# Optimization experiments

Hardware: AMD Instinct MI355X
Metric: run time of the kernel (lower is better)

The kernel has to match this reference:

```python
import jax, jax.numpy as jnp
import numpy as np

B, H, E, L = 2048, 4096, 8, 512
TAU = 1.0


def setup_inputs() -> dict:
    key = jax.random.key(0)
    k1, k2, k3, k4 = jax.random.split(key, 4)
    hidden = jax.random.normal(k1, (B, H), dtype=jnp.float32)
    envs = jax.random.normal(k2, (B, E), dtype=jnp.float32)
    idx = jnp.arange(B, dtype=jnp.int64)
    gumbel = jax.random.gumbel(k3, (B, E), dtype=jnp.float32)
    W = jax.random.normal(k4, (E, L, H), dtype=jnp.float32) * (1.0 / np.sqrt(H))
    return {"hidden": hidden, "envs": envs, "idx": idx, "gumbel": gumbel, "W": W}


def _hard_gumbel_softmax(log_probs, gumbel, tau):
    # F.gumbel_softmax(log_probs, tau=1, hard=True) with pre-sampled gumbel noise
    y_soft = jax.nn.softmax((log_probs + gumbel) / tau, axis=-1)
    y_hard = jax.nn.one_hot(jnp.argmax(y_soft, axis=-1), y_soft.shape[-1], dtype=y_soft.dtype)
    # straight-through estimator
    return y_hard + y_soft - jax.lax.stop_gradient(y_soft)


def reference(hidden, envs, idx, gumbel, W):
    # gating: env = gumbel_softmax(log_softmax(envs[idx]))  -> [B, E]
    log_probs = jax.nn.log_softmax(envs[idx], axis=-1)
    env = _hard_gumbel_softmax(log_probs, gumbel, TAU)
    # per-expert logits: [B, E, L]; fuses the per-sample python loop
    expert_logits = jnp.einsum("bh,elh->bel", hidden, W)
    # gating combine: [B, L]
    logits = jnp.einsum("be,bel->bl", env, expert_logits)
    # variance penalty over expert weights
    W_mean = jnp.mean(W, axis=0)  # [L, H]
    diff_sq = jnp.sum((W - W_mean[None]) ** 2, axis=(1, 2))  # ||W_e - W_mean||_2^2 per expert
    l1 = jnp.sum(jnp.abs(W), axis=(1, 2))                    # ||W_e||_1 per expert
    loss_penalty = jnp.mean(diff_sq / (l1 ** 2))
    return logits, loss_penalty
```

## Files before the change

kernel.cpp:

```cpp
#include <hip/hip_runtime.h>
#include <hip/hip_bf16.h>

constexpr int B = 2048, H = 4096, E = 8, L = 512;
constexpr int LH = L * H;

typedef float f4v __attribute__((ext_vector_type(4)));
typedef short short8 __attribute__((ext_vector_type(8)));

constexpr int BT = 128;
constexpr int LT = 128;
constexpr int KT = 32;
constexpr int SK = 4;
constexpr int RTMAX = 3;
constexpr int NITER = (H / SK) / KT;

constexpr int NGEMM = 4 * 2 * 4 * 4 * RTMAX;
constexpr int NPEN = 2048;

constexpr size_t WS_COUNTS = 0;
constexpr size_t WS_ACCUM = 32;
constexpr size_t WS_ROWLIST = 96;
constexpr size_t WS_ZERO_BYTES = 96;

using as1_u32 = const __attribute__((address_space(1))) unsigned int;
using as3_u32 = __attribute__((address_space(3))) unsigned int;

static __device__ __forceinline__ void dma16(const float* g, float* lds) {
  __builtin_amdgcn_global_load_lds((as1_u32*)g, (as3_u32*)lds, 16, 0, 0);
}

static __device__ __forceinline__ unsigned pk2(float a, float b) {
  __hip_bfloat162 p = __float22bfloat162_rn(make_float2(a, b));
  unsigned u;
  __builtin_memcpy(&u, &p, 4);
  return u;
}

static __device__ __forceinline__ short8 cvt8(f4v lo, f4v hi) {
  union { short8 s; unsigned u[4]; } r;
  r.u[0] = pk2(lo.x, lo.y);
  r.u[1] = pk2(lo.z, lo.w);
  r.u[2] = pk2(hi.x, hi.y);
  r.u[3] = pk2(hi.z, hi.w);
  return r.s;
}

__global__ void gating_kernel(const float* __restrict__ envs,
                              const float* __restrict__ gumbel,
                              int* __restrict__ counts,
                              int* __restrict__ row_list) {
  int b = blockIdx.x * blockDim.x + threadIdx.x;
  if (b >= B) return;
  float zmax = -1e30f;
  int am = 0;
#pragma unroll
  for (int e = 0; e < E; ++e) {
    float z = envs[b * E + e] + gumbel[b * E + e];
    if (z > zmax) { zmax = z; am = e; }
  }
  int pos = atomicAdd(&counts[am], 1);
  row_list[am * B + pos] = b;
}

__launch_bounds__(256, 2)
__global__ void fused_kernel(const float* __restrict__ hidden,
                             const float* __restrict__ W,
                             const int* __restrict__ counts,
                             const int* __restrict__ row_list,
                             float* __restrict__ out,
                             float* __restrict__ accum) {
  const int id = blockIdx.x;
  const int t = threadIdx.x;

  __shared__ __align__(16) float AshF[2][BT * KT];
  __shared__ __align__(16) float BshF[2][LT * KT];
  __shared__ int rlsh[BT];
  __shared__ float red[4][16];

  if (id >= NGEMM) {
    const int p = (id - NGEMM) * 256 + t;

    float4 w[E];
    float mx = 0.f, my = 0.f, mz = 0.f, mw = 0.f;
#pragma unroll
    for (int e = 0; e < E; ++e) {
      w[e] = *(const float4*)(W + (size_t)e * LH + (size_t)p * 4);
      mx += w[e].x; my += w[e].y; mz += w[e].z; mw += w[e].w;
    }
    mx *= 0.125f; my *= 0.125f; mz *= 0.125f; mw *= 0.125f;

    float vals[16];
#pragma unroll
    for (int e = 0; e < E; ++e) {
      float dx = w[e].x - mx, dy = w[e].y - my, dz = w[e].z - mz,
            dw = w[e].w - mw;
      vals[e] = dx * dx + dy * dy + dz * dz + dw * dw;
      vals[8 + e] =
          fabsf(w[e].x) + fabsf(w[e].y) + fabsf(w[e].z) + fabsf(w[e].w);
    }
#pragma unroll
    for (int k = 0; k < 16; ++k) {
      float v = vals[k];
      for (int off = 32; off > 0; off >>= 1) v += __shfl_xor(v, off);
      vals[k] = v;
    }
    const int wv = t >> 6, lane = t & 63;
    if (lane == 0) {
#pragma unroll
      for (int k = 0; k < 16; ++k) red[wv][k] = vals[k];
    }
    __syncthreads();
    if (t < 16) {
      atomicAdd(&accum[t], red[0][t] + red[1][t] + red[2][t] + red[3][t]);
    }
    return;
  }

  const int lt = id & 3;
  const int ep = (id >> 2) & 1;
  const int sk = (id >> 3) & 3;
  const int eh = (id >> 5) & 3;
  const int rt = id >> 7;
  const int e = eh * 2 + ep;

  const int cnt = counts[e];
  const int rbase = rt * BT;
  if (rbase >= cnt) return;
  const int lbase = lt * LT;

  if (t < BT) {
    int rr = rbase + t;
    rlsh[t] = row_list[e * B + (rr < cnt ? rr : (cnt - 1))];
  }
  __syncthreads();

  const float* Wp = W + (size_t)e * LH + (size_t)lbase * H;

  const int wave = t >> 6;
  const int lane = t & 63;
  const int quad = lane >> 4;
  const int l16 = lane & 15;
  const int wm = (wave >> 1) * 64;
  const int wn = (wave & 1) * 64;

  const int kbeg = sk * (H / SK);
  const int srow = lane >> 3;
  const int sblk = lane & 7;

  const float* sp[8];
  float* sl[2][8];
  const bool stageA = (wave < 2);
#pragma unroll
  for (int i = 0; i < 8; ++i) {
    int r = (stageA ? wave : (wave - 2)) * 64 + i * 8 + srow;
    int gblk = sblk ^ (r & 7);
    if (stageA) {
      sp[i] = hidden + (size_t)rlsh[r] * H + kbeg + gblk * 4;
      sl[0][i] = &AshF[0][(r - srow) * KT];
      sl[1][i] = &AshF[1][(r - srow) * KT];
    } else {
      sp[i] = Wp + (size_t)r * H + kbeg + gblk * 4;
      sl[0][i] = &BshF[0][(r - srow) * KT];
      sl[1][i] = &BshF[1][(r - srow) * KT];
    }
  }

  auto stage = [&](int buf) {
#pragma unroll
    for (int i = 0; i < 8; ++i) {
      dma16(sp[i], sl[buf][i]);
      sp[i] += KT;
    }
  };

  const int r7 = l16 & 7;
  const int slo = (2 * quad) ^ r7;
  const int shi = slo ^ 1;

  f4v acc[4][4] = {};

  stage(0);

  for (int it = 0; it < NITER; ++it) {
    const int buf = it & 1;
    __syncthreads();
    if (it + 1 < NITER) stage(buf ^ 1);

    short8 af[4], bf[4];
#pragma unroll
    for (int i = 0; i < 4; ++i) {
      int ra = wm + i * 16 + l16;
      f4v lo = *(const f4v*)&AshF[buf][ra * KT + slo * 4];
      f4v hi = *(const f4v*)&AshF[buf][ra * KT + shi * 4];
      af[i] = cvt8(lo, hi);
    }
#pragma unroll
    for (int j = 0; j < 4; ++j) {
      int rb = wn + j * 16 + l16;
      f4v lo = *(const f4v*)&BshF[buf][rb * KT + slo * 4];
      f4v hi = *(const f4v*)&BshF[buf][rb * KT + shi * 4];
      bf[j] = cvt8(lo, hi);
    }
#pragma unroll
    for (int i = 0; i < 4; ++i)
#pragma unroll
      for (int j = 0; j < 4; ++j)
        acc[i][j] =
            __builtin_amdgcn_mfma_f32_16x16x32_bf16(af[i], bf[j], acc[i][j],
                                                    0, 0, 0);
  }

#pragma unroll
  for (int i = 0; i < 4; ++i) {
#pragma unroll
    for (int j = 0; j < 4; ++j) {
#pragma unroll
      for (int reg = 0; reg < 4; ++reg) {
        int rloc = wm + i * 16 + quad * 4 + reg;
        if (rbase + rloc < cnt) {
          int bidx = rlsh[rloc];
          atomicAdd(&out[(size_t)bidx * L + lbase + wn + j * 16 + l16],
                    acc[i][j][reg]);
        }
      }
    }
  }
}

__global__ void finalize_kernel(const float* __restrict__ accum,
                                float* __restrict__ out) {
  if (threadIdx.x == 0) {
    float loss = 0.f;
#pragma unroll
    for (int e = 0; e < E; ++e) {
      float l1 = accum[8 + e];
      loss += accum[e] / (l1 * l1);
    }
    out[(size_t)B * L] = loss * 0.125f;
  }
}

extern "C" void kernel_launch(void* const* d_in, const int* in_sizes, int n_in,
                              void* d_out, int out_size, void* d_ws, size_t ws_size,
                              hipStream_t stream) {
  (void)in_sizes; (void)n_in; (void)ws_size;
  const float* hidden = (const float*)d_in[0];
  const float* envs   = (const float*)d_in[1];
  const float* gumbel = (const float*)d_in[3];
  const float* W      = (const float*)d_in[4];
  float* out = (float*)d_out;

  char* ws = (char*)d_ws;
  int*   counts   = (int*)(ws + WS_COUNTS);
  float* accum    = (float*)(ws + WS_ACCUM);
  int*   row_list = (int*)(ws + WS_ROWLIST);

  (void)hipMemsetAsync(d_ws, 0, WS_ZERO_BYTES, stream);
  (void)hipMemsetAsync(d_out, 0, (size_t)out_size * sizeof(float), stream);

  gating_kernel<<<dim3(B / 256), dim3(256), 0, stream>>>(envs, gumbel, counts,
                                                         row_list);

  fused_kernel<<<dim3(NGEMM + NPEN), dim3(256), 0, stream>>>(
      hidden, W, counts, row_list, out, accum);

  finalize_kernel<<<dim3(1), dim3(64), 0, stream>>>(accum, out);
}
```

Measured before the change: 180.8 us.

## Halve row tile, interleave GEMM and penalty blocks, raise occupancy

The row tile drops from 128 to 64 and the maximum row-tile count doubles, so expert GEMM work is split into finer blocks that pad less against the uneven per-expert row counts. GEMM blocks and the W-penalty reduction blocks are interleaved in a 3:8 pattern across the grid so both run at the same time instead of the penalty blocks trailing at the end. Launch bounds move to 3 blocks per SM with smaller accumulators, and the DMA staging is redistributed across all four waves. In exchange, each block reuses its W tile across fewer rows, which raises W traffic and the number of atomic adds to the output.

```diff
diff --git a/kernel.cpp b/kernel.cpp
--- a/kernel.cpp
+++ b/kernel.cpp
@@ -7,15 +7,17 @@
 typedef float f4v __attribute__((ext_vector_type(4)));
 typedef short short8 __attribute__((ext_vector_type(8)));
 
-constexpr int BT = 128;
+constexpr int BT = 64;
 constexpr int LT = 128;
 constexpr int KT = 32;
 constexpr int SK = 4;
-constexpr int RTMAX = 3;
+constexpr int RTMAX = 6;
 constexpr int NITER = (H / SK) / KT;
 
 constexpr int NGEMM = 4 * 2 * 4 * 4 * RTMAX;
 constexpr int NPEN = 2048;
+
+constexpr int NGRID = NGEMM + NPEN;
 
 constexpr size_t WS_COUNTS = 0;
 constexpr size_t WS_ACCUM = 32;
@@ -62,7 +64,7 @@
   row_list[am * B + pos] = b;
 }
 
-__launch_bounds__(256, 2)
+__launch_bounds__(256, 3)
 __global__ void fused_kernel(const float* __restrict__ hidden,
                              const float* __restrict__ W,
                              const int* __restrict__ counts,
@@ -77,8 +79,12 @@
   __shared__ int rlsh[BT];
   __shared__ float red[4][16];
 
-  if (id >= NGEMM) {
-    const int p = (id - NGEMM) * 256 + t;
+  const int grp = id / 11;
+  const int rem = id - grp * 11;
+  const bool is_gemm = (rem < 3);
+
+  if (!is_gemm) {
+    const int p = (grp * 8 + (rem - 3)) * 256 + t;
 
     float4 w[E];
     float mx = 0.f, my = 0.f, mz = 0.f, mw = 0.f;
@@ -116,11 +122,12 @@
     return;
   }
 
-  const int lt = id & 3;
-  const int ep = (id >> 2) & 1;
-  const int sk = (id >> 3) & 3;
-  const int eh = (id >> 5) & 3;
-  const int rt = id >> 7;
+  const int gidx = grp * 3 + rem;
+  const int lt = gidx & 3;
+  const int ep = (gidx >> 2) & 1;
+  const int sk = (gidx >> 3) & 3;
+  const int eh = (gidx >> 5) & 3;
+  const int rt = gidx >> 7;
   const int e = eh * 2 + ep;
 
   const int cnt = counts[e];
@@ -140,34 +147,35 @@
   const int lane = t & 63;
   const int quad = lane >> 4;
   const int l16 = lane & 15;
-  const int wm = (wave >> 1) * 64;
+  const int wm = (wave >> 1) * 32;
   const int wn = (wave & 1) * 64;
 
   const int kbeg = sk * (H / SK);
   const int srow = lane >> 3;
   const int sblk = lane & 7;
-
-  const float* sp[8];
-  float* sl[2][8];
-  const bool stageA = (wave < 2);
-#pragma unroll
-  for (int i = 0; i < 8; ++i) {
-    int r = (stageA ? wave : (wave - 2)) * 64 + i * 8 + srow;
-    int gblk = sblk ^ (r & 7);
-    if (stageA) {
-      sp[i] = hidden + (size_t)rlsh[r] * H + kbeg + gblk * 4;
-      sl[0][i] = &AshF[0][(r - srow) * KT];
-      sl[1][i] = &AshF[1][(r - srow) * KT];
+  const int gblk = sblk ^ srow;
+
+  const float* sp[6];
+  float* sl[2][6];
+#pragma unroll
+  for (int i = 0; i < 6; ++i) {
+    int g = wave * 6 + i;
+    if (g < 8) {
+      int rr = g * 8 + srow;
+      sp[i] = hidden + (size_t)rlsh[rr] * H + kbeg + gblk * 4;
+      sl[0][i] = &AshF[0][g * 8 * KT];
+      sl[1][i] = &AshF[1][g * 8 * KT];
     } else {
-      sp[i] = Wp + (size_t)r * H + kbeg + gblk * 4;
-      sl[0][i] = &BshF[0][(r - srow) * KT];
-      sl[1][i] = &BshF[1][(r - srow) * KT];
+      int rb = (g - 8) * 8 + srow;
+      sp[i] = Wp + (size_t)rb * H + kbeg + gblk * 4;
+      sl[0][i] = &BshF[0][(g - 8) * 8 * KT];
+      sl[1][i] = &BshF[1][(g - 8) * 8 * KT];
     }
   }
 
   auto stage = [&](int buf) {
 #pragma unroll
-    for (int i = 0; i < 8; ++i) {
+    for (int i = 0; i < 6; ++i) {
       dma16(sp[i], sl[buf][i]);
       sp[i] += KT;
     }
@@ -177,7 +185,7 @@
   const int slo = (2 * quad) ^ r7;
   const int shi = slo ^ 1;
 
-  f4v acc[4][4] = {};
+  f4v acc[2][4] = {};
 
   stage(0);
 
@@ -186,9 +194,9 @@
     __syncthreads();
     if (it + 1 < NITER) stage(buf ^ 1);
 
-    short8 af[4], bf[4];
-#pragma unroll
-    for (int i = 0; i < 4; ++i) {
+    short8 af[2], bf[4];
+#pragma unroll
+    for (int i = 0; i < 2; ++i) {
       int ra = wm + i * 16 + l16;
       f4v lo = *(const f4v*)&AshF[buf][ra * KT + slo * 4];
       f4v hi = *(const f4v*)&AshF[buf][ra * KT + shi * 4];
@@ -202,7 +210,7 @@
       bf[j] = cvt8(lo, hi);
     }
 #pragma unroll
-    for (int i = 0; i < 4; ++i)
+    for (int i = 0; i < 2; ++i)
 #pragma unroll
       for (int j = 0; j < 4; ++j)
         acc[i][j] =
@@ -211,7 +219,7 @@
   }
 
 #pragma unroll
-  for (int i = 0; i < 4; ++i) {
+  for (int i = 0; i < 2; ++i) {
 #pragma unroll
     for (int j = 0; j < 4; ++j) {
 #pragma unroll
@@ -261,8 +269,8 @@
   gating_kernel<<<dim3(B / 256), dim3(256), 0, stream>>>(envs, gumbel, counts,
                                                          row_list);
 
-  fused_kernel<<<dim3(NGEMM + NPEN), dim3(256), 0, stream>>>(
-      hidden, W, counts, row_list, out, accum);
+  fused_kernel<<<dim3(NGRID), dim3(256), 0, stream>>>(hidden, W, counts,
+                                                      row_list, out, accum);
 
   finalize_kernel<<<dim3(1), dim3(64), 0, stream>>>(accum, out);
 }
```

Result: slower. 195.1 us (+7.9%).

## Double split-K and interleave penalty blocks with GEMM blocks in grid

Applied to the files above, without the earlier changes.

Raises the split-K factor from 4 to 8, doubling the number of GEMM tiles and halving each tile's K loop. Penalty work moves into grid-stride blocks (1536 instead of 2048) that are interleaved 16-per-8 with GEMM blocks, so both kinds of block run at the same time instead of all penalty blocks being dispatched after the GEMM ones. The aim is better load balance and occupancy across CUs, since many GEMM blocks exit early when an expert has few rows. The cost is twice as many atomic adds into the output and a shorter pipeline in each block.

```diff
diff --git a/kernel.cpp b/kernel.cpp
--- a/kernel.cpp
+++ b/kernel.cpp
@@ -10,12 +10,13 @@
 constexpr int BT = 128;
 constexpr int LT = 128;
 constexpr int KT = 32;
-constexpr int SK = 4;
+constexpr int SK = 8;
 constexpr int RTMAX = 3;
 constexpr int NITER = (H / SK) / KT;
 
-constexpr int NGEMM = 4 * 2 * 4 * 4 * RTMAX;
-constexpr int NPEN = 2048;
+constexpr int NGEMM = 4 * 2 * 8 * 4 * RTMAX;
+constexpr int NPEN = 96 * 16;
+constexpr int NGRID = 96 * 24;
 
 constexpr size_t WS_COUNTS = 0;
 constexpr size_t WS_ACCUM = 32;
@@ -77,27 +78,38 @@
   __shared__ int rlsh[BT];
   __shared__ float red[4][16];
 
-  if (id >= NGEMM) {
-    const int p = (id - NGEMM) * 256 + t;
-
-    float4 w[E];
-    float mx = 0.f, my = 0.f, mz = 0.f, mw = 0.f;
-#pragma unroll
-    for (int e = 0; e < E; ++e) {
-      w[e] = *(const float4*)(W + (size_t)e * LH + (size_t)p * 4);
-      mx += w[e].x; my += w[e].y; mz += w[e].z; mw += w[e].w;
-    }
-    mx *= 0.125f; my *= 0.125f; mz *= 0.125f; mw *= 0.125f;
+  const int grp = id / 24;
+  const int rem = id - grp * 24;
+
+  if (rem >= 8) {
+    const int pidx = grp * 16 + (rem - 8);
+
+    float dacc[E], lacc[E];
+#pragma unroll
+    for (int e = 0; e < E; ++e) { dacc[e] = 0.f; lacc[e] = 0.f; }
+
+    for (int p = pidx * 256 + t; p < LH / 4; p += NPEN * 256) {
+      float4 w[E];
+      float mx = 0.f, my = 0.f, mz = 0.f, mw = 0.f;
+#pragma unroll
+      for (int e = 0; e < E; ++e) {
+        w[e] = *(const float4*)(W + (size_t)e * LH + (size_t)p * 4);
+        mx += w[e].x; my += w[e].y; mz += w[e].z; mw += w[e].w;
+      }
+      mx *= 0.125f; my *= 0.125f; mz *= 0.125f; mw *= 0.125f;
+#pragma unroll
+      for (int e = 0; e < E; ++e) {
+        float dx = w[e].x - mx, dy = w[e].y - my, dz = w[e].z - mz,
+              dw = w[e].w - mw;
+        dacc[e] += dx * dx + dy * dy + dz * dz + dw * dw;
+        lacc[e] +=
+            fabsf(w[e].x) + fabsf(w[e].y) + fabsf(w[e].z) + fabsf(w[e].w);
+      }
+    }
 
     float vals[16];
 #pragma unroll
-    for (int e = 0; e < E; ++e) {
-      float dx = w[e].x - mx, dy = w[e].y - my, dz = w[e].z - mz,
-            dw = w[e].w - mw;
-      vals[e] = dx * dx + dy * dy + dz * dz + dw * dw;
-      vals[8 + e] =
-          fabsf(w[e].x) + fabsf(w[e].y) + fabsf(w[e].z) + fabsf(w[e].w);
-    }
+    for (int e = 0; e < E; ++e) { vals[e] = dacc[e]; vals[8 + e] = lacc[e]; }
 #pragma unroll
     for (int k = 0; k < 16; ++k) {
       float v = vals[k];
@@ -116,11 +128,12 @@
     return;
   }
 
-  const int lt = id & 3;
-  const int ep = (id >> 2) & 1;
-  const int sk = (id >> 3) & 3;
-  const int eh = (id >> 5) & 3;
-  const int rt = id >> 7;
+  const int gidx = grp * 8 + rem;
+  const int lt = gidx & 3;
+  const int ep = (gidx >> 2) & 1;
+  const int sk = (gidx >> 3) & 7;
+  const int eh = (gidx >> 6) & 3;
+  const int rt = gidx >> 8;
   const int e = eh * 2 + ep;
 
   const int cnt = counts[e];
@@ -261,8 +274,8 @@
   gating_kernel<<<dim3(B / 256), dim3(256), 0, stream>>>(envs, gumbel, counts,
                                                          row_list);
 
-  fused_kernel<<<dim3(NGEMM + NPEN), dim3(256), 0, stream>>>(
-      hidden, W, counts, row_list, out, accum);
+  fused_kernel<<<dim3(NGRID), dim3(256), 0, stream>>>(hidden, W, counts,
+                                                      row_list, out, accum);
 
   finalize_kernel<<<dim3(1), dim3(64), 0, stream>>>(accum, out);
 }
```

Result: slower. 193.9 us (+7.2%).

## Interleave penalty reduction into GEMM blocks instead of separate penalty blocks

Applied to the files above, without the earlier changes.

Removes the 2048 dedicated penalty-reduction blocks and spreads the W variance/L1 work across the GEMM blocks. Each block loads a strip of W during even GEMM iterations and accumulates during odd ones. Blocks that have no GEMM rows process their share directly. The aim is to hide the penalty's memory traffic under MFMA compute and avoid extra block launches, at the cost of more register pressure in the GEMM loop and load imbalance, since every block now carries a penalty share.

```diff
diff --git a/kernel.cpp b/kernel.cpp
--- a/kernel.cpp
+++ b/kernel.cpp
@@ -15,7 +15,10 @@
 constexpr int NITER = (H / SK) / KT;
 
 constexpr int NGEMM = 4 * 2 * 4 * 4 * RTMAX;
-constexpr int NPEN = 2048;
+
+constexpr int Q = LH / 4;
+constexpr int QSHARE = (Q + NGEMM - 1) / NGEMM;
+constexpr int NSTRIP = (QSHARE + 255) / 256;
 
 constexpr size_t WS_COUNTS = 0;
 constexpr size_t WS_ACCUM = 32;
@@ -77,27 +80,43 @@
   __shared__ int rlsh[BT];
   __shared__ float red[4][16];
 
-  if (id >= NGEMM) {
-    const int p = (id - NGEMM) * 256 + t;
-
-    float4 w[E];
+  const int q0 = id * QSHARE;
+  const int share = (Q - q0 < QSHARE) ? (Q - q0) : QSHARE;
+  float dacc[E], lacc[E];
+#pragma unroll
+  for (int e = 0; e < E; ++e) { dacc[e] = 0.f; lacc[e] = 0.f; }
+
+  float4 pw[E];
+  float pv = 0.f;
+
+  auto pen_issue = [&](int s) {
+    int off = s * 256 + t;
+    pv = (off < share) ? 1.f : 0.f;
+    int p = q0 + ((off < share) ? off : 0);
+#pragma unroll
+    for (int e = 0; e < E; ++e)
+      pw[e] = *(const float4*)(W + (size_t)e * LH + (size_t)p * 4);
+  };
+  auto pen_consume = [&]() {
     float mx = 0.f, my = 0.f, mz = 0.f, mw = 0.f;
 #pragma unroll
     for (int e = 0; e < E; ++e) {
-      w[e] = *(const float4*)(W + (size_t)e * LH + (size_t)p * 4);
-      mx += w[e].x; my += w[e].y; mz += w[e].z; mw += w[e].w;
+      mx += pw[e].x; my += pw[e].y; mz += pw[e].z; mw += pw[e].w;
     }
     mx *= 0.125f; my *= 0.125f; mz *= 0.125f; mw *= 0.125f;
-
+#pragma unroll
+    for (int e = 0; e < E; ++e) {
+      float dx = pw[e].x - mx, dy = pw[e].y - my, dz = pw[e].z - mz,
+            dw = pw[e].w - mw;
+      dacc[e] += pv * (dx * dx + dy * dy + dz * dz + dw * dw);
+      lacc[e] += pv * (fabsf(pw[e].x) + fabsf(pw[e].y) + fabsf(pw[e].z) +
+                       fabsf(pw[e].w));
+    }
+  };
+  auto pen_reduce = [&]() {
     float vals[16];
 #pragma unroll
-    for (int e = 0; e < E; ++e) {
-      float dx = w[e].x - mx, dy = w[e].y - my, dz = w[e].z - mz,
-            dw = w[e].w - mw;
-      vals[e] = dx * dx + dy * dy + dz * dz + dw * dw;
-      vals[8 + e] =
-          fabsf(w[e].x) + fabsf(w[e].y) + fabsf(w[e].z) + fabsf(w[e].w);
-    }
+    for (int e = 0; e < E; ++e) { vals[e] = dacc[e]; vals[8 + e] = lacc[e]; }
 #pragma unroll
     for (int k = 0; k < 16; ++k) {
       float v = vals[k];
@@ -113,8 +132,7 @@
     if (t < 16) {
       atomicAdd(&accum[t], red[0][t] + red[1][t] + red[2][t] + red[3][t]);
     }
-    return;
-  }
+  };
 
   const int lt = id & 3;
   const int ep = (id >> 2) & 1;
@@ -125,7 +143,16 @@
 
   const int cnt = counts[e];
   const int rbase = rt * BT;
-  if (rbase >= cnt) return;
+
+  if (rbase >= cnt) {
+#pragma unroll
+    for (int s = 0; s < NSTRIP; ++s) {
+      pen_issue(s);
+      pen_consume();
+    }
+    pen_reduce();
+    return;
+  }
   const int lbase = lt * LT;
 
   if (t < BT) {
@@ -186,6 +213,8 @@
     __syncthreads();
     if (it + 1 < NITER) stage(buf ^ 1);
 
+    if (!(it & 1) && (it >> 1) < NSTRIP) pen_issue(it >> 1);
+
     short8 af[4], bf[4];
 #pragma unroll
     for (int i = 0; i < 4; ++i) {
@@ -201,6 +230,9 @@
       f4v hi = *(const f4v*)&BshF[buf][rb * KT + shi * 4];
       bf[j] = cvt8(lo, hi);
     }
+
+    if ((it & 1) && (it >> 1) < NSTRIP) pen_consume();
+
 #pragma unroll
     for (int i = 0; i < 4; ++i)
 #pragma unroll
@@ -225,6 +257,9 @@
       }
     }
   }
+
+  __syncthreads();
+  pen_reduce();
 }
 
 __global__ void finalize_kernel(const float* __restrict__ accum,
@@ -261,8 +296,8 @@
   gating_kernel<<<dim3(B / 256), dim3(256), 0, stream>>>(envs, gumbel, counts,
                                                          row_list);
 
-  fused_kernel<<<dim3(NGEMM + NPEN), dim3(256), 0, stream>>>(
-      hidden, W, counts, row_list, out, accum);
+  fused_kernel<<<dim3(NGEMM), dim3(256), 0, stream>>>(hidden, W, counts,
+                                                      row_list, out, accum);
 
   finalize_kernel<<<dim3(1), dim3(64), 0, stream>>>(accum, out);
 }
```

After: 187.8 us. 3.9% more time.
